# Optimization experiments

Measured on AMD Instinct MI355X. Metric: run time of the kernel, lower is better.

## Reference

```python
import jax, jax.numpy as jnp
import numpy as np

B, N, D, H = 4, 1024, 1024, 16
Dh = D // H


def setup_inputs() -> dict:
    key = jax.random.key(0)
    ks = jax.random.split(key, 5)
    w = 0.02
    return {
        "x": jax.random.normal(ks[0], (B, N, D), dtype=jnp.float32),
        "Wq": jax.random.normal(ks[1], (D, D), dtype=jnp.float32) * w,
        "bq": jnp.zeros((D,), dtype=jnp.float32),
        "Wk": jax.random.normal(ks[2], (D, D), dtype=jnp.float32) * w,
        "bk": jnp.zeros((D,), dtype=jnp.float32),
        "Wv": jax.random.normal(ks[3], (D, D), dtype=jnp.float32) * w,
        "bv": jnp.zeros((D,), dtype=jnp.float32),
        "Wc": jax.random.normal(ks[4], (D, D), dtype=jnp.float32) * w,
        "bc": jnp.zeros((D,), dtype=jnp.float32),
    }


def reference(x, Wq, bq, Wk, bk, Wv, bv, Wc, bc):
    # q/k/v projections: nn.Linear computes x @ W.T + b
    q = jnp.einsum("bnd,ed->bne", x, Wq) + bq
    k = jnp.einsum("bnd,ed->bne", x, Wk) + bk
    v = jnp.einsum("bnd,ed->bne", x, Wv) + bv
    # split heads: [B,N,D] -> [B,H,N,Dh]
    qh = q.reshape(B, N, H, Dh).transpose(0, 2, 1, 3)
    kh = k.reshape(B, N, H, Dh).transpose(0, 2, 1, 3)
    vh = v.reshape(B, N, H, Dh).transpose(0, 2, 1, 3)
    # NOTE (faithful quirk): original uses scale = q.size(1) = seq_len N,
    # not head_dim, so scores are scaled by N**-0.5.
    scale = jnp.float32(N) ** -0.5
    scores = jnp.einsum("bhnd,bhmd->bhnm", qh, kh) * scale  # [B,H,N,N]
    attn = jax.nn.softmax(scores, axis=-1)
    # attn_dropout = 0.0 -> identity
    o = jnp.einsum("bhnm,bhmd->bhnd", attn, vh)  # [B,H,N,Dh]
    # NOTE (faithful quirk): original does v.resize(original_size) on the
    # contiguous [B,H,N,Dh] tensor, reinterpreting memory as [B,N,D]
    # WITHOUT permuting heads back. Replicate exactly:
    o = o.reshape(B, N, D)
    out = jnp.einsum("bnd,ed->bne", o, Wc) + bc
    return out
```

## Files before the change

kernel.cpp:

```cpp
#include <hip/hip_runtime.h>
#include <cstddef>
#include <cstdint>

#define B_  4
#define N_  1024
#define D_  1024
#define H_  16
#define DH  64
#define M_  4096

typedef __attribute__((ext_vector_type(4))) float   f32x4;
typedef __attribute__((ext_vector_type(8))) __bf16  bf16x8;

#define MFMA(a, b, c) __builtin_amdgcn_mfma_f32_16x16x32_bf16((a), (b), (c), 0, 0, 0)
#define GLDS(gp, lp) __builtin_amdgcn_global_load_lds( \
    (__attribute__((address_space(1))) void*)(gp),     \
    (__attribute__((address_space(3))) void*)(lp), 16, 0, 0)

__global__ __launch_bounds__(256) void convert_k(
    const float* __restrict__ x,  const float* __restrict__ Wq,
    const float* __restrict__ Wk, const float* __restrict__ Wv,
    const float* __restrict__ Wc,
    __bf16* __restrict__ xb, __bf16* __restrict__ wqkvb,
    __bf16* __restrict__ wcb)
{
    const unsigned u = blockIdx.x * 256u + threadIdx.x;
    const unsigned e = u * 8u;
    const float* src;
    __bf16* dst;
    if (e < 4194304u) { src = x + e; dst = xb + e; }
    else {
        const unsigned t2 = e - 4194304u;
        const unsigned wsel = t2 >> 20;
        const unsigned wo = t2 & 1048575u;
        src = (wsel == 0 ? Wq : wsel == 1 ? Wk : wsel == 2 ? Wv : Wc) + wo;
        dst = (wsel < 3 ? wqkvb + (size_t)wsel * 1048576u : wcb) + wo;
    }
    const float4 f0 = *(const float4*)(src);
    const float4 f1 = *(const float4*)(src + 4);
    bf16x8 r;
    r[0] = (__bf16)f0.x; r[1] = (__bf16)f0.y; r[2] = (__bf16)f0.z; r[3] = (__bf16)f0.w;
    r[4] = (__bf16)f1.x; r[5] = (__bf16)f1.y; r[6] = (__bf16)f1.z; r[7] = (__bf16)f1.w;
    *(bf16x8*)dst = r;
}

__global__ __launch_bounds__(512, 2) void gemm_qkv256(
    const __bf16* __restrict__ xb, const __bf16* __restrict__ Wb,
    const float* __restrict__ bq, const float* __restrict__ bk,
    const float* __restrict__ bv,
    __bf16* __restrict__ qk_out, __bf16* __restrict__ vT)
{
    __shared__ __bf16 ring[65536];

    const int tid  = threadIdx.x;
    const int w    = tid >> 6;
    const int lane = tid & 63;
    const int quad = lane >> 4;
    const int l15  = lane & 15;
    const int wr   = w >> 2;
    const int wc   = w & 3;

    const int bid = blockIdx.x;
    const bool VT = (bid >= 128);
    int m0, n0;
    const __bf16 *Ap, *Bp;
    if (!VT) { m0 = (bid >> 3) * 256; n0 = (bid & 7) * 256; Ap = xb; Bp = Wb; }
    else {
        const int v = bid - 128;
        m0 = (v & 3) * 256;
        n0 = (v >> 2) * 256;
        Ap = Wb + (size_t)2 * D_ * D_; Bp = xb;
    }

    const size_t sgl = (size_t)(w * 16 + l15) * D_ + quad * 8;
    const __bf16* Asrc = Ap + (size_t)m0 * D_ + sgl;
    const __bf16* Bsrc = Bp + (size_t)n0 * D_ + sgl;
    __bf16* const ringA = ring;
    __bf16* const ringB = ring + 32768;
    const int sdst = w * 1024;

#define STG_A(tt, h) do {                                               \
    const __bf16* s_ = Asrc + (size_t)(h) * 128 * D_ + (tt) * 64;       \
    __bf16* d_ = ringA + ((((tt) & 1) * 2 + (h)) * 8192) + sdst;        \
    GLDS(s_, d_); GLDS(s_ + 32, d_ + 512); } while (0)
#define STG_B(tt, h) do {                                               \
    const __bf16* s_ = Bsrc + (size_t)(h) * 128 * D_ + (tt) * 64;       \
    __bf16* d_ = ringB + ((((tt) & 1) * 2 + (h)) * 8192) + sdst;        \
    GLDS(s_, d_); GLDS(s_ + 32, d_ + 512); } while (0)

    f32x4 acc[8][4];
    #pragma unroll
    for (int i = 0; i < 8; ++i)
        #pragma unroll
        for (int j = 0; j < 4; ++j)
            acc[i][j] = (f32x4){0.f, 0.f, 0.f, 0.f};

    STG_B(0, 0); STG_B(0, 1);
    STG_A(0, 0); STG_A(0, 1);
    STG_B(1, 0); STG_B(1, 1);

    const int rdo = lane * 8;

#define READ_A(q)                                                       \
    afr[0][0] = *(const bf16x8*)(Asl + ((2*(q)  )*2 + 0)*512);          \
    afr[0][1] = *(const bf16x8*)(Asl + ((2*(q)  )*2 + 1)*512);          \
    afr[1][0] = *(const bf16x8*)(Asl + ((2*(q)+1)*2 + 0)*512);          \
    afr[1][1] = *(const bf16x8*)(Asl + ((2*(q)+1)*2 + 1)*512);

#define PHASE_MFMA(q)                                                   \
    __builtin_amdgcn_s_barrier();                                       \
    asm volatile("s_waitcnt lgkmcnt(0)" ::: "memory");                  \
    __builtin_amdgcn_s_setprio(1);                                      \
    _Pragma("unroll")                                                   \
    for (int i = 0; i < 2; ++i)                                         \
      _Pragma("unroll")                                                 \
      for (int nt = 0; nt < 4; ++nt) {                                  \
        acc[2*(q)+i][nt] = MFMA(afr[i][0], bfr[nt][0], acc[2*(q)+i][nt]); \
        acc[2*(q)+i][nt] = MFMA(afr[i][1], bfr[nt][1], acc[2*(q)+i][nt]); \
      }                                                                 \
    __builtin_amdgcn_s_setprio(0);

    for (int t = 0; t < 16; ++t) {
        if (t < 15) asm volatile("s_waitcnt vmcnt(4)" ::: "memory");
        else        asm volatile("s_waitcnt vmcnt(0)" ::: "memory");
        __builtin_amdgcn_s_barrier();

        const __bf16* Asl = ringA + ((t & 1) * 2 + wr) * 8192 + rdo;
        const __bf16* Bsl = ringB + ((t & 1) * 2 + (wc >> 1)) * 8192
                                  + (wc & 1) * 4096 + rdo;
        bf16x8 afr[2][2], bfr[4][2];

        if (t < 15) STG_A(t + 1, 0);
        #pragma unroll
        for (int nt = 0; nt < 4; ++nt) {
            bfr[nt][0] = *(const bf16x8*)(Bsl + (nt * 2 + 0) * 512);
            bfr[nt][1] = *(const bf16x8*)(Bsl + (nt * 2 + 1) * 512);
        }
        READ_A(0)
        PHASE_MFMA(0)
        __builtin_amdgcn_s_barrier();

        if (t < 15) STG_A(t + 1, 1);
        READ_A(1)
        PHASE_MFMA(1)
        __builtin_amdgcn_s_barrier();

        if (t < 14) STG_B(t + 2, 0);
        READ_A(2)
        PHASE_MFMA(2)
        __builtin_amdgcn_s_barrier();

        if (t < 14) STG_B(t + 2, 1);
        READ_A(3)
        PHASE_MFMA(3)
    }
#undef STG_A
#undef STG_B
#undef READ_A
#undef PHASE_MFMA

    if (!VT) {
        const int zq = n0 >> 10;
        const float* bias = zq ? bk : bq;
        const int nb = (n0 & 1023) + wc * 64;
        float bvv[4];
        #pragma unroll
        for (int nt = 0; nt < 4; ++nt) bvv[nt] = bias[nb + nt * 16 + l15];
        __bf16* C = qk_out + (size_t)zq * M_ * D_;
        #pragma unroll
        for (int mt = 0; mt < 8; ++mt) {
            #pragma unroll
            for (int r = 0; r < 4; ++r) {
                const int row = m0 + wr * 128 + mt * 16 + quad * 4 + r;
                #pragma unroll
                for (int nt = 0; nt < 4; ++nt) {
                    const int col = nb + nt * 16 + l15;
                    const size_t idx = (((size_t)(row >> 10) * H_ + (col >> 6)) * N_
                                        + (row & 1023)) * DH + (col & 63);
                    C[idx] = (__bf16)(acc[mt][nt][r] + bvv[nt]);
                }
            }
        }
    } else {
        #pragma unroll
        for (int mt = 0; mt < 8; ++mt) {
            #pragma unroll
            for (int r = 0; r < 4; ++r) {
                const int row = m0 + wr * 128 + mt * 16 + quad * 4 + r;
                const float brow = bv[row];
                #pragma unroll
                for (int nt = 0; nt < 4; ++nt) {
                    const int col = n0 + wc * 64 + nt * 16 + l15;
                    const size_t idx = (((size_t)(col >> 10) * H_ + (row >> 6)) * DH
                                        + (row & 63)) * N_ + (col & 1023);
                    vT[idx] = (__bf16)(acc[mt][nt][r] + brow);
                }
            }
        }
    }
}

__global__ __launch_bounds__(256, 6) void gemm_out(
    const __bf16* __restrict__ A0, const __bf16* __restrict__ Wb,
    const float* __restrict__ b0, float* __restrict__ Cb)
{
    __shared__ __bf16 As[2048];
    __shared__ __bf16 Bs[4096];

    const int tid  = threadIdx.x;
    const int w    = tid >> 6;
    const int lane = tid & 63;
    const int quad = lane >> 4;
    const int l15  = lane & 15;
    const int wr   = w >> 1, wc = w & 1;

    const int m0 = blockIdx.y * 64;
    const int n0 = blockIdx.x * 128;

    const int Tt = tid >> 6, ko = (tid >> 4) & 3, l = tid & 15;
    const size_t aoff  = (size_t)(m0 + Tt * 16 + l) * D_ + ko * 8;
    const size_t boff1 = (size_t)(n0 + Tt * 16 + l) * D_ + ko * 8;
    const size_t boff2 = boff1 + (size_t)64 * D_;
    __bf16* adst  = As + w * 512;
    __bf16* bdst1 = Bs + w * 512;
    __bf16* bdst2 = Bs + 2048 + w * 512;

    f32x4 acc[2][4];
    #pragma unroll
    for (int i = 0; i < 2; ++i)
        #pragma unroll
        for (int j = 0; j < 4; ++j)
            acc[i][j] = (f32x4){0.f, 0.f, 0.f, 0.f};

    for (int k0 = 0; k0 < D_; k0 += 32) {
        GLDS(A0 + aoff  + k0, adst);
        GLDS(Wb + boff1 + k0, bdst1);
        GLDS(Wb + boff2 + k0, bdst2);
        __syncthreads();

        bf16x8 af[2], bf[4];
        #pragma unroll
        for (int mt = 0; mt < 2; ++mt)
            af[mt] = *(const bf16x8*)(As + (((wr * 2 + mt) * 4 + quad) * 16 + l15) * 8);
        #pragma unroll
        for (int nt = 0; nt < 4; ++nt)
            bf[nt] = *(const bf16x8*)(Bs + (((wc * 4 + nt) * 4 + quad) * 16 + l15) * 8);
        #pragma unroll
        for (int mt = 0; mt < 2; ++mt)
            #pragma unroll
            for (int nt = 0; nt < 4; ++nt)
                acc[mt][nt] = MFMA(af[mt], bf[nt], acc[mt][nt]);
        __syncthreads();
    }

    float bvv[4];
    #pragma unroll
    for (int nt = 0; nt < 4; ++nt)
        bvv[nt] = b0[n0 + wc * 64 + nt * 16 + l15];
    #pragma unroll
    for (int mt = 0; mt < 2; ++mt) {
        #pragma unroll
        for (int r = 0; r < 4; ++r) {
            const int row = m0 + (wr * 2 + mt) * 16 + quad * 4 + r;
            #pragma unroll
            for (int nt = 0; nt < 4; ++nt) {
                const int col = n0 + wc * 64 + nt * 16 + l15;
                Cb[(size_t)row * D_ + col] = acc[mt][nt][r] + bvv[nt];
            }
        }
    }
}

#define SP  68
#define SC2 0.04508422f

__global__ __launch_bounds__(256, 4) void attn_mfma(
    const __bf16* __restrict__ qh, const __bf16* __restrict__ kh,
    const __bf16* __restrict__ vT, __bf16* __restrict__ ob)
{
    __shared__ __bf16 Ks[4096];
    __shared__ __bf16 Vs[4096];
    __shared__ float  Ps[4][16 * SP];

    const int tid  = threadIdx.x;
    const int w    = tid >> 6;
    const int lane = tid & 63;
    const int quad = lane >> 4;
    const int l15  = lane & 15;

    const int bh = blockIdx.x & 63;
    const int qt = blockIdx.x >> 6;
    const int b  = bh >> 4;
    const int h  = bh & 15;

    const __bf16* qp = qh + ((size_t)(b * H_ + h) * N_ + qt * 64 + w * 16 + l15) * DH + quad * 8;
    const bf16x8 qf0 = *(const bf16x8*)(qp);
    const bf16x8 qf1 = *(const bf16x8*)(qp + 32);

    const int c1 = tid, c2 = tid + 256;
    const int nt1 = c1 >> 7, ko1 = (c1 >> 4) & 7, l1 = c1 & 15;
    const int nt2 = c2 >> 7, ko2 = (c2 >> 4) & 7, l2 = c2 & 15;
    const __bf16* khead = kh + (size_t)(b * H_ + h) * N_ * DH;
    const __bf16* vhead = vT + (size_t)(b * H_ + h) * DH * N_;
    const size_t koff1 = (size_t)(nt1 * 16 + l1) * DH + ko1 * 8;
    const size_t koff2 = (size_t)(nt2 * 16 + l2) * DH + ko2 * 8;
    const size_t voff1 = (size_t)(nt1 * 16 + l1) * N_ + ko1 * 8;
    const size_t voff2 = (size_t)(nt2 * 16 + l2) * N_ + ko2 * 8;
    __bf16* ksdst1 = Ks + w * 512;
    __bf16* ksdst2 = Ks + 2048 + w * 512;
    __bf16* vsdst1 = Vs + w * 512;
    __bf16* vsdst2 = Vs + 2048 + w * 512;

    float psum[4] = {0.f, 0.f, 0.f, 0.f};
    f32x4 Ov[4];
    #pragma unroll
    for (int nt = 0; nt < 4; ++nt) Ov[nt] = (f32x4){0.f, 0.f, 0.f, 0.f};

    for (int kt = 0; kt < 16; ++kt) {
        GLDS(khead + (size_t)kt * 64 * DH + koff1, ksdst1);
        GLDS(khead + (size_t)kt * 64 * DH + koff2, ksdst2);
        GLDS(vhead + (size_t)kt * 64 + voff1, vsdst1);
        GLDS(vhead + (size_t)kt * 64 + voff2, vsdst2);
        __syncthreads();

        f32x4 sa[4];
        #pragma unroll
        for (int nt = 0; nt < 4; ++nt) {
            const bf16x8 kf0 = *(const bf16x8*)(Ks + (nt * 128 + quad * 16 + l15) * 8);
            const bf16x8 kf1 = *(const bf16x8*)(Ks + (nt * 128 + (quad + 4) * 16 + l15) * 8);
            sa[nt] = (f32x4){0.f, 0.f, 0.f, 0.f};
            sa[nt] = MFMA(qf0, kf0, sa[nt]);
            sa[nt] = MFMA(qf1, kf1, sa[nt]);
        }

        #pragma unroll
        for (int nt = 0; nt < 4; ++nt) {
            #pragma unroll
            for (int r = 0; r < 4; ++r) {
                const float p = __builtin_exp2f(sa[nt][r] * SC2);
                psum[r] += p;
                Ps[w][(quad * 4 + r) * SP + nt * 16 + l15] = p;
            }
        }

        #pragma unroll
        for (int kw = 0; kw < 2; ++kw) {
            const f32x4 pa = *(const f32x4*)&Ps[w][l15 * SP + kw * 32 + quad * 8];
            const f32x4 pb = *(const f32x4*)&Ps[w][l15 * SP + kw * 32 + quad * 8 + 4];
            bf16x8 pf;
            #pragma unroll
            for (int j = 0; j < 4; ++j) { pf[j] = (__bf16)pa[j]; pf[4 + j] = (__bf16)pb[j]; }
            #pragma unroll
            for (int nt = 0; nt < 4; ++nt) {
                const bf16x8 vf = *(const bf16x8*)(Vs + (nt * 128 + (kw * 4 + quad) * 16 + l15) * 8);
                Ov[nt] = MFMA(pf, vf, Ov[nt]);
            }
        }
        __syncthreads();
    }

    float lrow[4];
    #pragma unroll
    for (int r = 0; r < 4; ++r) {
        float lt = psum[r];
        lt += __shfl_xor(lt, 1);
        lt += __shfl_xor(lt, 2);
        lt += __shfl_xor(lt, 4);
        lt += __shfl_xor(lt, 8);
        lrow[r] = lt;
    }

    #pragma unroll
    for (int r = 0; r < 4; ++r) {
        const float inv = 1.0f / lrow[r];
        const int row = qt * 64 + w * 16 + quad * 4 + r;
        __bf16* op = ob + ((size_t)(b * H_ + h) * N_ + row) * DH + l15;
        #pragma unroll
        for (int nt = 0; nt < 4; ++nt)
            op[nt * 16] = (__bf16)(Ov[nt][r] * inv);
    }
}

extern "C" void kernel_launch(void* const* d_in, const int* in_sizes, int n_in,
                              void* d_out, int out_size, void* d_ws, size_t ws_size,
                              hipStream_t stream) {
    const float* x  = (const float*)d_in[0];
    const float* Wq = (const float*)d_in[1];
    const float* bq = (const float*)d_in[2];
    const float* Wk = (const float*)d_in[3];
    const float* bk = (const float*)d_in[4];
    const float* Wv = (const float*)d_in[5];
    const float* bv = (const float*)d_in[6];
    const float* Wc = (const float*)d_in[7];
    const float* bc = (const float*)d_in[8];
    float* out = (float*)d_out;

    char* base = (char*)d_ws;
    __bf16* xb    = (__bf16*)(base);
    __bf16* wqkvb = (__bf16*)(base + (size_t)8  * 1048576);
    __bf16* wcb   = (__bf16*)(base + (size_t)14 * 1048576);
    __bf16* qkvb  = (__bf16*)(base + (size_t)16 * 1048576);
    __bf16* vTb   = (__bf16*)(base + (size_t)40 * 1048576);
    __bf16* obf   = (__bf16*)(base);

    __bf16* qhb = qkvb;
    __bf16* khb = qkvb + (size_t)M_ * D_;

    convert_k<<<dim3(4096), dim3(256), 0, stream>>>(
        x, Wq, Wk, Wv, Wc, xb, wqkvb, wcb);

    gemm_qkv256<<<dim3(192), dim3(512), 0, stream>>>(
        xb, wqkvb, bq, bk, bv, qkvb, vTb);

    attn_mfma<<<dim3(1024), dim3(256), 0, stream>>>(qhb, khb, vTb, obf);

    gemm_out<<<dim3(8, 64, 1), dim3(256), 0, stream>>>(obf, wcb, bc, out);
}
```

Baseline: 194.0 us.

## Double-buffer K/V tiles in attention and fold softmax scale into Q

The attention kernel now double-buffers K and V tiles in LDS, prefetching the next tile while computing the current one and dropping the second barrier per iteration. The softmax scale is folded into Q during the projection epilogue, removing a multiply before each exp2. It also raises wave priority around the MFMA sections and lowers the occupancy hint from 4 to 3 to make room for the doubled LDS. Folding the scale before the bf16 rounding of Q changes numerics slightly, and the extra LDS may reduce occupancy.

```diff
diff --git a/kernel.cpp b/kernel.cpp
--- a/kernel.cpp
+++ b/kernel.cpp
@@ -8,6 +8,8 @@
 #define H_  16
 #define DH  64
 #define M_  4096
+
+#define SC2 0.04508422f
 
 typedef __attribute__((ext_vector_type(4))) float   f32x4;
 typedef __attribute__((ext_vector_type(8))) __bf16  bf16x8;
@@ -162,6 +164,7 @@
     if (!VT) {
         const int zq = n0 >> 10;
         const float* bias = zq ? bk : bq;
+        const float qs = zq ? 1.0f : SC2;
         const int nb = (n0 & 1023) + wc * 64;
         float bvv[4];
         #pragma unroll
@@ -177,7 +180,7 @@
                     const int col = nb + nt * 16 + l15;
                     const size_t idx = (((size_t)(row >> 10) * H_ + (col >> 6)) * N_
                                         + (row & 1023)) * DH + (col & 63);
-                    C[idx] = (__bf16)(acc[mt][nt][r] + bvv[nt]);
+                    C[idx] = (__bf16)((acc[mt][nt][r] + bvv[nt]) * qs);
                 }
             }
         }
@@ -272,14 +275,13 @@
 }
 
 #define SP  68
-#define SC2 0.04508422f
-
-__global__ __launch_bounds__(256, 4) void attn_mfma(
+
+__global__ __launch_bounds__(256, 3) void attn_mfma(
     const __bf16* __restrict__ qh, const __bf16* __restrict__ kh,
     const __bf16* __restrict__ vT, __bf16* __restrict__ ob)
 {
-    __shared__ __bf16 Ks[4096];
-    __shared__ __bf16 Vs[4096];
+    __shared__ __bf16 Ks[2 * 4096];
+    __shared__ __bf16 Vs[2 * 4096];
     __shared__ float  Ps[4][16 * SP];
 
     const int tid  = threadIdx.x;
@@ -306,43 +308,55 @@
     const size_t koff2 = (size_t)(nt2 * 16 + l2) * DH + ko2 * 8;
     const size_t voff1 = (size_t)(nt1 * 16 + l1) * N_ + ko1 * 8;
     const size_t voff2 = (size_t)(nt2 * 16 + l2) * N_ + ko2 * 8;
-    __bf16* ksdst1 = Ks + w * 512;
-    __bf16* ksdst2 = Ks + 2048 + w * 512;
-    __bf16* vsdst1 = Vs + w * 512;
-    __bf16* vsdst2 = Vs + 2048 + w * 512;
+
+#define STG_KV(kt, p) do {                                              \
+    const size_t kb_ = (size_t)(kt) * 64;                               \
+    GLDS(khead + kb_ * DH + koff1, Ks + (p) * 4096 + w * 512);          \
+    GLDS(khead + kb_ * DH + koff2, Ks + (p) * 4096 + 2048 + w * 512);   \
+    GLDS(vhead + kb_ + voff1,      Vs + (p) * 4096 + w * 512);          \
+    GLDS(vhead + kb_ + voff2,      Vs + (p) * 4096 + 2048 + w * 512);   \
+} while (0)
 
     float psum[4] = {0.f, 0.f, 0.f, 0.f};
     f32x4 Ov[4];
     #pragma unroll
     for (int nt = 0; nt < 4; ++nt) Ov[nt] = (f32x4){0.f, 0.f, 0.f, 0.f};
 
+    STG_KV(0, 0);
+
     for (int kt = 0; kt < 16; ++kt) {
-        GLDS(khead + (size_t)kt * 64 * DH + koff1, ksdst1);
-        GLDS(khead + (size_t)kt * 64 * DH + koff2, ksdst2);
-        GLDS(vhead + (size_t)kt * 64 + voff1, vsdst1);
-        GLDS(vhead + (size_t)kt * 64 + voff2, vsdst2);
-        __syncthreads();
+        asm volatile("s_waitcnt vmcnt(0)" ::: "memory");
+        __builtin_amdgcn_s_barrier();
+        asm volatile("" ::: "memory");
+
+        if (kt < 15) STG_KV(kt + 1, (kt + 1) & 1);
+
+        const __bf16* Kb = Ks + (kt & 1) * 4096;
+        const __bf16* Vb = Vs + (kt & 1) * 4096;
 
         f32x4 sa[4];
+        __builtin_amdgcn_s_setprio(1);
         #pragma unroll
         for (int nt = 0; nt < 4; ++nt) {
-            const bf16x8 kf0 = *(const bf16x8*)(Ks + (nt * 128 + quad * 16 + l15) * 8);
-            const bf16x8 kf1 = *(const bf16x8*)(Ks + (nt * 128 + (quad + 4) * 16 + l15) * 8);
+            const bf16x8 kf0 = *(const bf16x8*)(Kb + (nt * 128 + quad * 16 + l15) * 8);
+            const bf16x8 kf1 = *(const bf16x8*)(Kb + (nt * 128 + (quad + 4) * 16 + l15) * 8);
             sa[nt] = (f32x4){0.f, 0.f, 0.f, 0.f};
             sa[nt] = MFMA(qf0, kf0, sa[nt]);
             sa[nt] = MFMA(qf1, kf1, sa[nt]);
         }
+        __builtin_amdgcn_s_setprio(0);
 
         #pragma unroll
         for (int nt = 0; nt < 4; ++nt) {
             #pragma unroll
             for (int r = 0; r < 4; ++r) {
-                const float p = __builtin_exp2f(sa[nt][r] * SC2);
+                const float p = __builtin_exp2f(sa[nt][r]);
                 psum[r] += p;
                 Ps[w][(quad * 4 + r) * SP + nt * 16 + l15] = p;
             }
         }
 
+        __builtin_amdgcn_s_setprio(1);
         #pragma unroll
         for (int kw = 0; kw < 2; ++kw) {
             const f32x4 pa = *(const f32x4*)&Ps[w][l15 * SP + kw * 32 + quad * 8];
@@ -352,12 +366,13 @@
             for (int j = 0; j < 4; ++j) { pf[j] = (__bf16)pa[j]; pf[4 + j] = (__bf16)pb[j]; }
             #pragma unroll
             for (int nt = 0; nt < 4; ++nt) {
-                const bf16x8 vf = *(const bf16x8*)(Vs + (nt * 128 + (kw * 4 + quad) * 16 + l15) * 8);
+                const bf16x8 vf = *(const bf16x8*)(Vb + (nt * 128 + (kw * 4 + quad) * 16 + l15) * 8);
                 Ov[nt] = MFMA(pf, vf, Ov[nt]);
             }
         }
-        __syncthreads();
-    }
+        __builtin_amdgcn_s_setprio(0);
+    }
+#undef STG_KV
 
     float lrow[4];
     #pragma unroll
```

Result: slower. 204.8 us (+5.5%).

## Register-prefetch K/V tiles in attention and fold softmax scale into Q projection

Applied to the files above, without the earlier changes.

The attention kernel no longer loads K/V tiles with direct global-to-LDS loads. It now prefetches the next tile into registers while the current tile is computed, then writes it to LDS between two barriers. The softmax scale (with log2e) is applied to Q in the projection epilogue, so the per-element multiply before exp2 is removed. s_setprio calls are added around the MFMA sections to favour matrix work across waves. The extra register staging and LDS stores may lower occupancy or add LDS write traffic, and rounding scaled Q to bf16 changes numerics slightly.

```diff
diff --git a/kernel.cpp b/kernel.cpp
--- a/kernel.cpp
+++ b/kernel.cpp
@@ -8,6 +8,8 @@
 #define H_  16
 #define DH  64
 #define M_  4096
+
+#define SC2 0.04508422f
 
 typedef __attribute__((ext_vector_type(4))) float   f32x4;
 typedef __attribute__((ext_vector_type(8))) __bf16  bf16x8;
@@ -162,6 +164,7 @@
     if (!VT) {
         const int zq = n0 >> 10;
         const float* bias = zq ? bk : bq;
+        const float qs = zq ? 1.0f : SC2;
         const int nb = (n0 & 1023) + wc * 64;
         float bvv[4];
         #pragma unroll
@@ -177,7 +180,7 @@
                     const int col = nb + nt * 16 + l15;
                     const size_t idx = (((size_t)(row >> 10) * H_ + (col >> 6)) * N_
                                         + (row & 1023)) * DH + (col & 63);
-                    C[idx] = (__bf16)(acc[mt][nt][r] + bvv[nt]);
+                    C[idx] = (__bf16)((acc[mt][nt][r] + bvv[nt]) * qs);
                 }
             }
         }
@@ -272,7 +275,6 @@
 }
 
 #define SP  68
-#define SC2 0.04508422f
 
 __global__ __launch_bounds__(256, 4) void attn_mfma(
     const __bf16* __restrict__ qh, const __bf16* __restrict__ kh,
@@ -306,24 +308,39 @@
     const size_t koff2 = (size_t)(nt2 * 16 + l2) * DH + ko2 * 8;
     const size_t voff1 = (size_t)(nt1 * 16 + l1) * N_ + ko1 * 8;
     const size_t voff2 = (size_t)(nt2 * 16 + l2) * N_ + ko2 * 8;
-    __bf16* ksdst1 = Ks + w * 512;
-    __bf16* ksdst2 = Ks + 2048 + w * 512;
-    __bf16* vsdst1 = Vs + w * 512;
-    __bf16* vsdst2 = Vs + 2048 + w * 512;
+
+    __bf16* const kw1 = Ks + w * 512 + lane * 8;
+    __bf16* const kw2 = Ks + 2048 + w * 512 + lane * 8;
+    __bf16* const vw1 = Vs + w * 512 + lane * 8;
+    __bf16* const vw2 = Vs + 2048 + w * 512 + lane * 8;
 
     float psum[4] = {0.f, 0.f, 0.f, 0.f};
     f32x4 Ov[4];
     #pragma unroll
     for (int nt = 0; nt < 4; ++nt) Ov[nt] = (f32x4){0.f, 0.f, 0.f, 0.f};
 
+    bf16x8 kr1 = *(const bf16x8*)(khead + koff1);
+    bf16x8 kr2 = *(const bf16x8*)(khead + koff2);
+    bf16x8 vr1 = *(const bf16x8*)(vhead + voff1);
+    bf16x8 vr2 = *(const bf16x8*)(vhead + voff2);
+
     for (int kt = 0; kt < 16; ++kt) {
-        GLDS(khead + (size_t)kt * 64 * DH + koff1, ksdst1);
-        GLDS(khead + (size_t)kt * 64 * DH + koff2, ksdst2);
-        GLDS(vhead + (size_t)kt * 64 + voff1, vsdst1);
-        GLDS(vhead + (size_t)kt * 64 + voff2, vsdst2);
         __syncthreads();
+        *(bf16x8*)kw1 = kr1;
+        *(bf16x8*)kw2 = kr2;
+        *(bf16x8*)vw1 = vr1;
+        *(bf16x8*)vw2 = vr2;
+        if (kt < 15) {
+            const size_t kb = (size_t)(kt + 1) * 64;
+            kr1 = *(const bf16x8*)(khead + kb * DH + koff1);
+            kr2 = *(const bf16x8*)(khead + kb * DH + koff2);
+            vr1 = *(const bf16x8*)(vhead + kb + voff1);
+            vr2 = *(const bf16x8*)(vhead + kb + voff2);
+        }
+        __syncthreads();
 
         f32x4 sa[4];
+        __builtin_amdgcn_s_setprio(1);
         #pragma unroll
         for (int nt = 0; nt < 4; ++nt) {
             const bf16x8 kf0 = *(const bf16x8*)(Ks + (nt * 128 + quad * 16 + l15) * 8);
@@ -332,17 +349,19 @@
             sa[nt] = MFMA(qf0, kf0, sa[nt]);
             sa[nt] = MFMA(qf1, kf1, sa[nt]);
         }
+        __builtin_amdgcn_s_setprio(0);
 
         #pragma unroll
         for (int nt = 0; nt < 4; ++nt) {
             #pragma unroll
             for (int r = 0; r < 4; ++r) {
-                const float p = __builtin_exp2f(sa[nt][r] * SC2);
+                const float p = __builtin_exp2f(sa[nt][r]);
                 psum[r] += p;
                 Ps[w][(quad * 4 + r) * SP + nt * 16 + l15] = p;
             }
         }
 
+        __builtin_amdgcn_s_setprio(1);
         #pragma unroll
         for (int kw = 0; kw < 2; ++kw) {
             const f32x4 pa = *(const f32x4*)&Ps[w][l15 * SP + kw * 32 + quad * 8];
@@ -356,7 +375,7 @@
                 Ov[nt] = MFMA(pf, vf, Ov[nt]);
             }
         }
-        __syncthreads();
+        __builtin_amdgcn_s_setprio(0);
     }
 
     float lrow[4];
```

Measured after the change: 193.3 us. About the same (-0.4%).
